# Kernel tuning notes

Hardware: AMD Instinct MI355X
Metric: run time of the kernel (lower is better)

Reference implementation:

```python
import jax, jax.numpy as jnp
import numpy as np

B, S, E = 2, 2048, 2048
H = 16
D = E // H  # head_dim = 128
ROPE_BASE = 10000.0


def _rope(x):
    # x: [B, H, S, D], rotate-half RoPE with offset=0
    half = D // 2
    inv_freq = 1.0 / (ROPE_BASE ** (jnp.arange(0, half, dtype=jnp.float32) * 2.0 / D))
    pos = jnp.arange(x.shape[2], dtype=jnp.float32)
    ang = pos[:, None] * inv_freq[None, :]          # [S, D/2]
    cos = jnp.cos(ang)[None, None, :, :]
    sin = jnp.sin(ang)[None, None, :, :]
    x1, x2 = x[..., :half], x[..., half:]
    return jnp.concatenate([x1 * cos - x2 * sin, x1 * sin + x2 * cos], axis=-1)


def setup_inputs() -> dict:
    key = jax.random.key(0)
    ks = jax.random.split(key, 9)
    sc = 1.0 / np.sqrt(E)
    inp = {
        'x': jax.random.normal(ks[0], (B, S, E), dtype=jnp.float32),
        'wq': jax.random.normal(ks[1], (E, E), dtype=jnp.float32) * sc,
        'bq': jax.random.normal(ks[2], (E,), dtype=jnp.float32) * 0.01,
        'wk': jax.random.normal(ks[3], (E, E), dtype=jnp.float32) * sc,
        'bk': jax.random.normal(ks[4], (E,), dtype=jnp.float32) * 0.01,
        'wv': jax.random.normal(ks[5], (E, E), dtype=jnp.float32) * sc,
        'bv': jax.random.normal(ks[6], (E,), dtype=jnp.float32) * 0.01,
        'wo': jax.random.normal(ks[7], (E, E), dtype=jnp.float32) * sc,
        'bo': jax.random.normal(ks[8], (E,), dtype=jnp.float32) * 0.01,
        'causal_mask': jnp.triu(jnp.ones((S, S), dtype=bool), k=1),  # True = masked
        'attention_mask': jnp.zeros((B, S), dtype=bool),             # True = padding
    }
    return inp


def reference(x, wq, bq, wk, bk, wv, bv, wo, bo, causal_mask, attention_mask):
    # nn.Linear: y = x @ W.T + b
    q = (x @ wq.T + bq).reshape(B, S, H, D).transpose(0, 2, 1, 3)  # [B,H,S,D]
    k = (x @ wk.T + bk).reshape(B, S, H, D).transpose(0, 2, 1, 3)
    v = (x @ wv.T + bv).reshape(B, S, H, D).transpose(0, 2, 1, 3)
    q = _rope(q)
    k = _rope(k)
    scores = jnp.einsum('bhsd,bhtd->bhst', q, k) / jnp.sqrt(jnp.float32(D))
    neg_inf = jnp.float32(-jnp.inf)
    scores = jnp.where(causal_mask[None, None, :, :], neg_inf, scores)
    scores = jnp.where(attention_mask[:, None, None, :], neg_inf, scores)
    attn = jax.nn.softmax(scores, axis=-1)
    out = jnp.einsum('bhst,bhtd->bhsd', attn, v)        # [B,H,S,D]
    out = out.transpose(0, 2, 1, 3).reshape(B, S, E)
    return out @ wo.T + bo
```

## Files before the change

### kernel.cpp

```cpp
#include <hip/hip_runtime.h>

#define BATCH 2
#define SEQ   2048
#define EMB   2048
#define NH    16
#define HD    128

typedef unsigned short u16;
typedef u16 u16x8 __attribute__((ext_vector_type(8)));
typedef __bf16 bf16x8 __attribute__((ext_vector_type(8)));
typedef float f32x4 __attribute__((ext_vector_type(4)));

__device__ __forceinline__ u16 f2bf(float f) {
  union { float f; unsigned u; } v; v.f = f;
  unsigned r = v.u + 0x7FFFu + ((v.u >> 16) & 1u);
  return (u16)(r >> 16);
}
__device__ __forceinline__ float bf2f(u16 b) {
  union { unsigned u; float f; } v; v.u = ((unsigned)b) << 16;
  return v.f;
}
__device__ __forceinline__ void gload_lds16(const u16* g, u16* l) {
  __builtin_amdgcn_global_load_lds(
      (__attribute__((address_space(1))) void*)(void*)g,
      (__attribute__((address_space(3))) void*)(void*)l, 16, 0, 0);
}

__global__ void cvt_f32_bf16(const float* __restrict__ in, u16* __restrict__ out, int n) {
  int i = (blockIdx.x * 256 + threadIdx.x) * 4;
  const int stride = gridDim.x * 256 * 4;
  for (; i + 3 < n; i += stride) {
    float4 v = *(const float4*)(in + i);
    u16 o0 = f2bf(v.x), o1 = f2bf(v.y), o2 = f2bf(v.z), o3 = f2bf(v.w);
    unsigned lo = (unsigned)o0 | ((unsigned)o1 << 16);
    unsigned hi = (unsigned)o2 | ((unsigned)o3 << 16);
    uint2 pack; pack.x = lo; pack.y = hi;
    *(uint2*)(out + i) = pack;
  }
}

__global__ void rope_table(float* __restrict__ cosT, float* __restrict__ sinT) {
  const int s = blockIdx.x;
  const int j = threadIdx.x;
  float inv = powf(10000.0f, -(float)j / 64.0f);
  float ang = (float)s * inv;
  cosT[s * 64 + j] = cosf(ang);
  sinT[s * 64 + j] = sinf(ang);
}

__global__ void rope_apply(u16* __restrict__ q, const float* __restrict__ cosT,
                           const float* __restrict__ sinT) {
  const int idx = blockIdx.x * 256 + threadIdx.x;
  const int j = idx & 63;
  const int s = (idx >> 6) & (SEQ - 1);
  const int bh = idx >> 17;
  u16* base = q + ((long)bh * SEQ + s) * HD;
  float x1 = bf2f(base[j]), x2 = bf2f(base[j + 64]);
  float c = cosT[s * 64 + j], sn = sinT[s * 64 + j];
  base[j]      = f2bf(x1 * c - x2 * sn);
  base[j + 64] = f2bf(x1 * sn + x2 * c);
}

__global__ __launch_bounds__(256)
void transpose_v(const u16* __restrict__ in, u16* __restrict__ out) {
  __shared__ u16 T[64 * 72];
  const int tid = threadIdx.x;
  const int s0 = blockIdx.x * 64, d0 = blockIdx.y * 64, bh = blockIdx.z;
  const int r = tid >> 2, c = tid & 3;
  const u16* ip = in + ((long)bh * SEQ + s0 + r) * HD + d0 + c * 16;
  *(u16x8*)&T[r * 72 + c * 16]     = *(const u16x8*)ip;
  *(u16x8*)&T[r * 72 + c * 16 + 8] = *(const u16x8*)(ip + 8);
  __syncthreads();
  u16* op = out + ((long)bh * HD + d0 + r) * SEQ + s0 + c * 16;
  u16x8 a, b;
#pragma unroll
  for (int e = 0; e < 8; ++e) a[e] = T[(c * 16 + e) * 72 + r];
#pragma unroll
  for (int e = 0; e < 8; ++e) b[e] = T[(c * 16 + 8 + e) * 72 + r];
  *(u16x8*)op = a;
  *(u16x8*)(op + 8) = b;
}

template <int MODE>
__global__ __launch_bounds__(256)
void gemm_bt(const u16* __restrict__ A, const u16* __restrict__ Bw,
             const float* __restrict__ bias, void* __restrict__ out,
             int M, int N, int K) {
  __shared__ u16 As[128 * 32];
  __shared__ u16 Bs[128 * 32];
  const int tid = threadIdx.x;
  const int wave = tid >> 6, lane = tid & 63;
  const int lr = lane & 15, lk = lane >> 4;
  const int m0 = blockIdx.y * 128, n0 = blockIdx.x * 128;
  const int wr = (wave >> 1) * 64, wc = (wave & 1) * 64;
  f32x4 acc[4][4] = {};
  for (int kt = 0; kt < K; kt += 32) {
#pragma unroll
    for (int c = 0; c < 2; ++c) {
      int idx = c * 256 + tid;
      int row = idx >> 2, col = (idx & 3) * 8;
      gload_lds16(A + (long)(m0 + row) * K + kt + col, As + idx * 8);
      gload_lds16(Bw + (long)(n0 + row) * K + kt + col, Bs + idx * 8);
    }
    __syncthreads();
    bf16x8 af[4], bfv[4];
#pragma unroll
    for (int m = 0; m < 4; ++m)
      af[m] = *(const bf16x8*)&As[(wr + m * 16 + lr) * 32 + lk * 8];
#pragma unroll
    for (int n = 0; n < 4; ++n)
      bfv[n] = *(const bf16x8*)&Bs[(wc + n * 16 + lr) * 32 + lk * 8];
#pragma unroll
    for (int m = 0; m < 4; ++m)
#pragma unroll
      for (int n = 0; n < 4; ++n)
        acc[m][n] = __builtin_amdgcn_mfma_f32_16x16x32_bf16(af[m], bfv[n], acc[m][n], 0, 0, 0);
    __syncthreads();
  }
#pragma unroll
  for (int n = 0; n < 4; ++n) {
    const int col = n0 + wc + n * 16 + lr;
    const float bb = bias[col];
#pragma unroll
    for (int m = 0; m < 4; ++m) {
      const int rbase = m0 + wr + m * 16 + lk * 4;
#pragma unroll
      for (int i = 0; i < 4; ++i) {
        const int row = rbase + i;
        const float val = acc[m][n][i] + bb;
        if (MODE == 0) {
          const int b = row >> 11, s = row & (SEQ - 1);
          const int h = col >> 7, d = col & (HD - 1);
          ((u16*)out)[(((long)(b * NH + h)) * SEQ + s) * HD + d] = f2bf(val);
        } else {
          ((float*)out)[(long)row * EMB + col] = val;
        }
      }
    }
  }
}

__global__ __launch_bounds__(256)
void attn_fwd(const u16* __restrict__ Q, const u16* __restrict__ K,
              const u16* __restrict__ Vt, u16* __restrict__ O) {
  __shared__ u16 Ks[64 * 128];
  __shared__ u16 Vts[128 * 64];
  __shared__ u16 Ps[4][16 * 72];
  const int tid = threadIdx.x, wave = tid >> 6, lane = tid & 63;
  const int lr = lane & 15, lk = lane >> 4;
  const int bh = blockIdx.y;
  const int qt = gridDim.x - 1 - blockIdx.x;
  const int qs = qt * 64;
  const long hoff = (long)bh * SEQ * HD;
  const u16* qb = Q + hoff + (long)(qs + wave * 16) * HD;

  bf16x8 qf[4];
#pragma unroll
  for (int ks = 0; ks < 4; ++ks)
    qf[ks] = *(const bf16x8*)(qb + (long)lr * HD + ks * 32 + lk * 8);

  f32x4 o[8] = {};
  float m_run[4] = {-1e30f, -1e30f, -1e30f, -1e30f};
  float l_run[4] = {0.f, 0.f, 0.f, 0.f};
  const float scale = 0.08838834764831845f;

  for (int t0 = 0; t0 <= qs; t0 += 64) {
#pragma unroll
    for (int c = 0; c < 4; ++c) {
      int i = c * 256 + tid;
      int row = i >> 4, cc = i & 15;
      int sc_ = cc ^ (row & 7);
      gload_lds16(K + hoff + (long)(t0 + row) * HD + sc_ * 8, Ks + i * 8);
    }
#pragma unroll
    for (int c = 0; c < 4; ++c) {
      int i = c * 256 + tid;
      int row = i >> 3, cc = i & 7;
      int sc_ = cc ^ (row & 7);
      gload_lds16(Vt + hoff + (long)row * SEQ + t0 + sc_ * 8, Vts + i * 8);
    }
    __syncthreads();

    f32x4 sc[4] = {};
#pragma unroll
    for (int tc = 0; tc < 4; ++tc) {
      const int rr = tc * 16 + lr;
#pragma unroll
      for (int ks = 0; ks < 4; ++ks) {
        bf16x8 kb = *(const bf16x8*)&Ks[rr * 128 + (((ks << 2) + lk) ^ (lr & 7)) * 8];
        sc[tc] = __builtin_amdgcn_mfma_f32_16x16x32_bf16(qf[ks], kb, sc[tc], 0, 0, 0);
      }
    }

    const bool diag = (t0 == qs);
    float rmax[4] = {-1e30f, -1e30f, -1e30f, -1e30f};
#pragma unroll
    for (int tc = 0; tc < 4; ++tc)
#pragma unroll
      for (int i = 0; i < 4; ++i) {
        float v = sc[tc][i] * scale;
        if (diag) {
          int tg = t0 + tc * 16 + lr;
          int qg = qs + wave * 16 + lk * 4 + i;
          if (tg > qg) v = -1e30f;
        }
        sc[tc][i] = v;
        rmax[i] = fmaxf(rmax[i], v);
      }
#pragma unroll
    for (int off = 1; off < 16; off <<= 1)
#pragma unroll
      for (int i = 0; i < 4; ++i)
        rmax[i] = fmaxf(rmax[i], __shfl_xor(rmax[i], off, 64));

    float alpha[4], rsum[4];
#pragma unroll
    for (int i = 0; i < 4; ++i) {
      float mn = fmaxf(m_run[i], rmax[i]);
      alpha[i] = __expf(m_run[i] - mn);
      m_run[i] = mn;
      rsum[i] = 0.f;
    }
#pragma unroll
    for (int tc = 0; tc < 4; ++tc)
#pragma unroll
      for (int i = 0; i < 4; ++i) {
        float p = __expf(sc[tc][i] - m_run[i]);
        sc[tc][i] = p;
        rsum[i] += p;
      }
#pragma unroll
    for (int off = 1; off < 16; off <<= 1)
#pragma unroll
      for (int i = 0; i < 4; ++i)
        rsum[i] += __shfl_xor(rsum[i], off, 64);
#pragma unroll
    for (int i = 0; i < 4; ++i) l_run[i] = l_run[i] * alpha[i] + rsum[i];
#pragma unroll
    for (int dc = 0; dc < 8; ++dc)
#pragma unroll
      for (int i = 0; i < 4; ++i) o[dc][i] *= alpha[i];

    u16* pw = Ps[wave];
#pragma unroll
    for (int tc = 0; tc < 4; ++tc)
#pragma unroll
      for (int i = 0; i < 4; ++i)
        pw[(lk * 4 + i) * 72 + tc * 16 + lr] = f2bf(sc[tc][i]);
    asm volatile("s_waitcnt lgkmcnt(0)" ::: "memory");

#pragma unroll
    for (int ks2 = 0; ks2 < 2; ++ks2) {
      bf16x8 pa = *(const bf16x8*)&pw[lr * 72 + ks2 * 32 + lk * 8];
#pragma unroll
      for (int dc = 0; dc < 8; ++dc) {
        const int dv = dc * 16 + lr;
        bf16x8 vb = *(const bf16x8*)&Vts[dv * 64 + (((ks2 << 2) + lk) ^ (lr & 7)) * 8];
        o[dc] = __builtin_amdgcn_mfma_f32_16x16x32_bf16(pa, vb, o[dc], 0, 0, 0);
      }
    }
    __syncthreads();
  }

  const int b = bh >> 4, h = bh & 15;
#pragma unroll
  for (int i = 0; i < 4; ++i) {
    float inv = 1.0f / l_run[i];
    int s = qs + wave * 16 + lk * 4 + i;
    u16* orow = O + ((long)b * SEQ + s) * EMB + h * HD;
#pragma unroll
    for (int dc = 0; dc < 8; ++dc)
      orow[dc * 16 + lr] = f2bf(o[dc][i] * inv);
  }
}

extern "C" void kernel_launch(void* const* d_in, const int* in_sizes, int n_in,
                              void* d_out, int out_size, void* d_ws, size_t ws_size,
                              hipStream_t stream) {
  const float* x  = (const float*)d_in[0];
  const float* wq = (const float*)d_in[1];
  const float* bq = (const float*)d_in[2];
  const float* wk = (const float*)d_in[3];
  const float* bk = (const float*)d_in[4];
  const float* wv = (const float*)d_in[5];
  const float* bv = (const float*)d_in[6];
  const float* wo = (const float*)d_in[7];
  const float* bo = (const float*)d_in[8];
  float* out = (float*)d_out;

  char* ws = (char*)d_ws;
  u16* xb  = (u16*)(ws + 0);
  u16* wqb = (u16*)(ws + 16777216);
  u16* wkb = (u16*)(ws + 25165824);
  u16* wvb = (u16*)(ws + 33554432);
  u16* wob = (u16*)(ws + 41943040);
  u16* qr  = (u16*)(ws + 50331648);
  u16* kr  = (u16*)(ws + 67108864);
  u16* vr  = (u16*)(ws + 83886080);
  u16* ao  = (u16*)(ws + 100663296);
  float* cosT = (float*)(ws + 117440512);
  float* sinT = (float*)(ws + 117964800);
  u16* vtr = xb;

  cvt_f32_bf16<<<2048, 256, 0, stream>>>(x, xb, BATCH * SEQ * EMB);
  cvt_f32_bf16<<<1024, 256, 0, stream>>>(wq, wqb, EMB * EMB);
  cvt_f32_bf16<<<1024, 256, 0, stream>>>(wk, wkb, EMB * EMB);
  cvt_f32_bf16<<<1024, 256, 0, stream>>>(wv, wvb, EMB * EMB);
  cvt_f32_bf16<<<1024, 256, 0, stream>>>(wo, wob, EMB * EMB);
  rope_table<<<SEQ, 64, 0, stream>>>(cosT, sinT);

  dim3 gg(EMB / 128, (BATCH * SEQ) / 128);
  gemm_bt<0><<<gg, 256, 0, stream>>>(xb, wqb, bq, qr, BATCH * SEQ, EMB, EMB);
  gemm_bt<0><<<gg, 256, 0, stream>>>(xb, wkb, bk, kr, BATCH * SEQ, EMB, EMB);
  gemm_bt<0><<<gg, 256, 0, stream>>>(xb, wvb, bv, vr, BATCH * SEQ, EMB, EMB);

  rope_apply<<<(BATCH * NH * SEQ * 64) / 256, 256, 0, stream>>>(qr, cosT, sinT);
  rope_apply<<<(BATCH * NH * SEQ * 64) / 256, 256, 0, stream>>>(kr, cosT, sinT);

  transpose_v<<<dim3(SEQ / 64, HD / 64, BATCH * NH), 256, 0, stream>>>(vr, vtr);

  attn_fwd<<<dim3(SEQ / 64, BATCH * NH), 256, 0, stream>>>(qr, kr, vtr, ao);

  gemm_bt<1><<<gg, 256, 0, stream>>>(ao, wob, bo, out, BATCH * SEQ, EMB, EMB);
}
```

Before: 601.5 us.

## Fuse QKV GEMMs and restructure attention with double buffering and lazy rescale

```diff
diff --git a/kernel.cpp b/kernel.cpp
--- a/kernel.cpp
+++ b/kernel.cpp
@@ -12,9 +12,8 @@
 typedef float f32x4 __attribute__((ext_vector_type(4)));
 
 __device__ __forceinline__ u16 f2bf(float f) {
-  union { float f; unsigned u; } v; v.f = f;
-  unsigned r = v.u + 0x7FFFu + ((v.u >> 16) & 1u);
-  return (u16)(r >> 16);
+  __bf16 h = (__bf16)f;
+  return __builtin_bit_cast(u16, h);
 }
 __device__ __forceinline__ float bf2f(u16 b) {
   union { unsigned u; float f; } v; v.u = ((unsigned)b) << 16;
@@ -84,7 +83,9 @@
 template <int MODE>
 __global__ __launch_bounds__(256)
 void gemm_bt(const u16* __restrict__ A, const u16* __restrict__ Bw,
-             const float* __restrict__ bias, void* __restrict__ out,
+             const float* __restrict__ b0, const float* __restrict__ b1,
+             const float* __restrict__ b2,
+             void* __restrict__ o0, void* __restrict__ o1, void* __restrict__ o2,
              int M, int N, int K) {
   __shared__ u16 As[128 * 32];
   __shared__ u16 Bs[128 * 32];
@@ -120,7 +121,11 @@
 #pragma unroll
   for (int n = 0; n < 4; ++n) {
     const int col = n0 + wc + n * 16 + lr;
-    const float bb = bias[col];
+    const int which = col >> 11;
+    const float* bias = (which == 0) ? b0 : (which == 1) ? b1 : b2;
+    const int cc = col & (EMB - 1);
+    const float bb = bias[cc];
+    void* outp = (which == 0) ? o0 : (which == 1) ? o1 : o2;
 #pragma unroll
     for (int m = 0; m < 4; ++m) {
       const int rbase = m0 + wr + m * 16 + lk * 4;
@@ -130,148 +135,177 @@
         const float val = acc[m][n][i] + bb;
         if (MODE == 0) {
           const int b = row >> 11, s = row & (SEQ - 1);
-          const int h = col >> 7, d = col & (HD - 1);
-          ((u16*)out)[(((long)(b * NH + h)) * SEQ + s) * HD + d] = f2bf(val);
+          const int h = cc >> 7, d = cc & (HD - 1);
+          ((u16*)outp)[(((long)(b * NH + h)) * SEQ + s) * HD + d] = f2bf(val);
         } else {
-          ((float*)out)[(long)row * EMB + col] = val;
+          ((float*)outp)[(long)row * EMB + col] = val;
         }
       }
     }
   }
+}
+
+#define THR_RAW 90.51f
+__device__ __forceinline__ void attn_tile(
+    const bf16x8 qf[4], f32x4 o[8], float m[4], float l[4],
+    const u16* __restrict__ Ksb, const u16* __restrict__ Vtsb,
+    u16* __restrict__ pw, int lr, int lk, int t0, int rowbase, bool diag) {
+  const float SC2 = 0.08838834764831845f * 1.4426950408889634f;
+  f32x4 sc[4] = {};
+#pragma unroll
+  for (int tc = 0; tc < 4; ++tc) {
+    const int rr = tc * 16 + lr;
+#pragma unroll
+    for (int ks = 0; ks < 4; ++ks) {
+      bf16x8 kb = *(const bf16x8*)&Ksb[rr * 128 + (((ks << 2) + lk) ^ (lr & 7)) * 8];
+      sc[tc] = __builtin_amdgcn_mfma_f32_16x16x32_bf16(qf[ks], kb, sc[tc], 0, 0, 0);
+    }
+  }
+  float rmax[4] = {-3e38f, -3e38f, -3e38f, -3e38f};
+#pragma unroll
+  for (int tc = 0; tc < 4; ++tc)
+#pragma unroll
+    for (int i = 0; i < 4; ++i) {
+      float v = sc[tc][i];
+      if (diag) {
+        int tg = t0 + tc * 16 + lr;
+        int qg = rowbase + lk * 4 + i;
+        if (tg > qg) v = -3e38f;
+        sc[tc][i] = v;
+      }
+      rmax[i] = fmaxf(rmax[i], v);
+    }
+#pragma unroll
+  for (int off = 1; off < 16; off <<= 1)
+#pragma unroll
+    for (int i = 0; i < 4; ++i)
+      rmax[i] = fmaxf(rmax[i], __shfl_xor(rmax[i], off, 64));
+
+  bool small = (rmax[0] <= m[0] + THR_RAW) && (rmax[1] <= m[1] + THR_RAW) &&
+               (rmax[2] <= m[2] + THR_RAW) && (rmax[3] <= m[3] + THR_RAW);
+  if (!__all(small)) {
+#pragma unroll
+    for (int i = 0; i < 4; ++i) {
+      float mn = fmaxf(m[i], rmax[i]);
+      float a = __builtin_amdgcn_exp2f((m[i] - mn) * SC2);
+      m[i] = mn;
+      l[i] *= a;
+#pragma unroll
+      for (int dc = 0; dc < 8; ++dc) o[dc][i] *= a;
+    }
+  }
+  float rsum[4] = {0.f, 0.f, 0.f, 0.f};
+#pragma unroll
+  for (int tc = 0; tc < 4; ++tc)
+#pragma unroll
+    for (int i = 0; i < 4; ++i) {
+      float p = __builtin_amdgcn_exp2f((sc[tc][i] - m[i]) * SC2);
+      sc[tc][i] = p;
+      rsum[i] += p;
+    }
+#pragma unroll
+  for (int off = 1; off < 16; off <<= 1)
+#pragma unroll
+    for (int i = 0; i < 4; ++i)
+      rsum[i] += __shfl_xor(rsum[i], off, 64);
+#pragma unroll
+  for (int i = 0; i < 4; ++i) l[i] += rsum[i];
+
+#pragma unroll
+  for (int tc = 0; tc < 4; ++tc)
+#pragma unroll
+    for (int i = 0; i < 4; ++i)
+      pw[(lk * 4 + i) * 72 + tc * 16 + lr] = f2bf(sc[tc][i]);
+  asm volatile("s_waitcnt lgkmcnt(0)" ::: "memory");
+#pragma unroll
+  for (int ks2 = 0; ks2 < 2; ++ks2) {
+    bf16x8 pa = *(const bf16x8*)&pw[lr * 72 + ks2 * 32 + lk * 8];
+#pragma unroll
+    for (int dc = 0; dc < 8; ++dc) {
+      const int dv = dc * 16 + lr;
+      bf16x8 vb = *(const bf16x8*)&Vtsb[dv * 64 + (((ks2 << 2) + lk) ^ (lr & 7)) * 8];
+      o[dc] = __builtin_amdgcn_mfma_f32_16x16x32_bf16(pa, vb, o[dc], 0, 0, 0);
+    }
+  }
+  asm volatile("s_waitcnt lgkmcnt(0)" ::: "memory");
 }
 
 __global__ __launch_bounds__(256)
 void attn_fwd(const u16* __restrict__ Q, const u16* __restrict__ K,
               const u16* __restrict__ Vt, u16* __restrict__ O) {
-  __shared__ u16 Ks[64 * 128];
-  __shared__ u16 Vts[128 * 64];
+  __shared__ u16 Ks[2][64 * 128];
+  __shared__ u16 Vts[2][128 * 64];
   __shared__ u16 Ps[4][16 * 72];
   const int tid = threadIdx.x, wave = tid >> 6, lane = tid & 63;
   const int lr = lane & 15, lk = lane >> 4;
   const int bh = blockIdx.y;
-  const int qt = gridDim.x - 1 - blockIdx.x;
-  const int qs = qt * 64;
+  const int qbi = gridDim.x - 1 - blockIdx.x;
+  const int q0 = qbi * 128;
   const long hoff = (long)bh * SEQ * HD;
-  const u16* qb = Q + hoff + (long)(qs + wave * 16) * HD;
-
-  bf16x8 qf[4];
-#pragma unroll
-  for (int ks = 0; ks < 4; ++ks)
-    qf[ks] = *(const bf16x8*)(qb + (long)lr * HD + ks * 32 + lk * 8);
-
-  f32x4 o[8] = {};
-  float m_run[4] = {-1e30f, -1e30f, -1e30f, -1e30f};
-  float l_run[4] = {0.f, 0.f, 0.f, 0.f};
-  const float scale = 0.08838834764831845f;
-
-  for (int t0 = 0; t0 <= qs; t0 += 64) {
-#pragma unroll
-    for (int c = 0; c < 4; ++c) {
-      int i = c * 256 + tid;
-      int row = i >> 4, cc = i & 15;
-      int sc_ = cc ^ (row & 7);
-      gload_lds16(K + hoff + (long)(t0 + row) * HD + sc_ * 8, Ks + i * 8);
-    }
-#pragma unroll
-    for (int c = 0; c < 4; ++c) {
-      int i = c * 256 + tid;
-      int row = i >> 3, cc = i & 7;
-      int sc_ = cc ^ (row & 7);
-      gload_lds16(Vt + hoff + (long)row * SEQ + t0 + sc_ * 8, Vts + i * 8);
-    }
+
+#define ATTN_STAGE(buf, tt0)                                                   \
+  do {                                                                         \
+    _Pragma("unroll") for (int c = 0; c < 4; ++c) {                            \
+      int i_ = c * 256 + tid;                                                  \
+      int kr_ = i_ >> 4, kc_ = i_ & 15;                                        \
+      gload_lds16(K + hoff + (long)((tt0) + kr_) * HD + (kc_ ^ (kr_ & 7)) * 8, \
+                  &Ks[buf][i_ * 8]);                                           \
+    }                                                                          \
+    _Pragma("unroll") for (int c = 0; c < 4; ++c) {                            \
+      int i_ = c * 256 + tid;                                                  \
+      int vr_ = i_ >> 3, vc_ = i_ & 7;                                         \
+      gload_lds16(Vt + hoff + (long)vr_ * SEQ + (tt0) + (vc_ ^ (vr_ & 7)) * 8, \
+                  &Vts[buf][i_ * 8]);                                          \
+    }                                                                          \
+  } while (0)
+
+  const int rbA = q0 + wave * 16;
+  const int rbB = q0 + 64 + wave * 16;
+  bf16x8 qfA[4], qfB[4];
+  {
+    const u16* qpA = Q + hoff + (long)rbA * HD + (long)lr * HD;
+    const u16* qpB = Q + hoff + (long)rbB * HD + (long)lr * HD;
+#pragma unroll
+    for (int ks = 0; ks < 4; ++ks) {
+      qfA[ks] = *(const bf16x8*)(qpA + ks * 32 + lk * 8);
+      qfB[ks] = *(const bf16x8*)(qpB + ks * 32 + lk * 8);
+    }
+  }
+
+  f32x4 oA[8] = {}, oB[8] = {};
+  float mA[4] = {-3e38f, -3e38f, -3e38f, -3e38f}, lA[4] = {0.f, 0.f, 0.f, 0.f};
+  float mB[4] = {-3e38f, -3e38f, -3e38f, -3e38f}, lB[4] = {0.f, 0.f, 0.f, 0.f};
+
+  const int nt = q0 / 64 + 2;
+  ATTN_STAGE(0, 0);
+  int cur = 0;
+  for (int ti = 0; ti < nt; ++ti) {
+    const int t0 = ti * 64;
     __syncthreads();
-
-    f32x4 sc[4] = {};
-#pragma unroll
-    for (int tc = 0; tc < 4; ++tc) {
-      const int rr = tc * 16 + lr;
-#pragma unroll
-      for (int ks = 0; ks < 4; ++ks) {
-        bf16x8 kb = *(const bf16x8*)&Ks[rr * 128 + (((ks << 2) + lk) ^ (lr & 7)) * 8];
-        sc[tc] = __builtin_amdgcn_mfma_f32_16x16x32_bf16(qf[ks], kb, sc[tc], 0, 0, 0);
-      }
-    }
-
-    const bool diag = (t0 == qs);
-    float rmax[4] = {-1e30f, -1e30f, -1e30f, -1e30f};
-#pragma unroll
-    for (int tc = 0; tc < 4; ++tc)
-#pragma unroll
-      for (int i = 0; i < 4; ++i) {
-        float v = sc[tc][i] * scale;
-        if (diag) {
-          int tg = t0 + tc * 16 + lr;
-          int qg = qs + wave * 16 + lk * 4 + i;
-          if (tg > qg) v = -1e30f;
-        }
-        sc[tc][i] = v;
-        rmax[i] = fmaxf(rmax[i], v);
-      }
-#pragma unroll
-    for (int off = 1; off < 16; off <<= 1)
-#pragma unroll
-      for (int i = 0; i < 4; ++i)
-        rmax[i] = fmaxf(rmax[i], __shfl_xor(rmax[i], off, 64));
-
-    float alpha[4], rsum[4];
-#pragma unroll
-    for (int i = 0; i < 4; ++i) {
-      float mn = fmaxf(m_run[i], rmax[i]);
-      alpha[i] = __expf(m_run[i] - mn);
-      m_run[i] = mn;
-      rsum[i] = 0.f;
-    }
-#pragma unroll
-    for (int tc = 0; tc < 4; ++tc)
-#pragma unroll
-      for (int i = 0; i < 4; ++i) {
-        float p = __expf(sc[tc][i] - m_run[i]);
-        sc[tc][i] = p;
-        rsum[i] += p;
-      }
-#pragma unroll
-    for (int off = 1; off < 16; off <<= 1)
-#pragma unroll
-      for (int i = 0; i < 4; ++i)
-        rsum[i] += __shfl_xor(rsum[i], off, 64);
-#pragma unroll
-    for (int i = 0; i < 4; ++i) l_run[i] = l_run[i] * alpha[i] + rsum[i];
-#pragma unroll
-    for (int dc = 0; dc < 8; ++dc)
-#pragma unroll
-      for (int i = 0; i < 4; ++i) o[dc][i] *= alpha[i];
-
+    if (ti + 1 < nt) ATTN_STAGE(cur ^ 1, t0 + 64);
     u16* pw = Ps[wave];
-#pragma unroll
-    for (int tc = 0; tc < 4; ++tc)
-#pragma unroll
-      for (int i = 0; i < 4; ++i)
-        pw[(lk * 4 + i) * 72 + tc * 16 + lr] = f2bf(sc[tc][i]);
-    asm volatile("s_waitcnt lgkmcnt(0)" ::: "memory");
-
-#pragma unroll
-    for (int ks2 = 0; ks2 < 2; ++ks2) {
-      bf16x8 pa = *(const bf16x8*)&pw[lr * 72 + ks2 * 32 + lk * 8];
-#pragma unroll
-      for (int dc = 0; dc < 8; ++dc) {
-        const int dv = dc * 16 + lr;
-        bf16x8 vb = *(const bf16x8*)&Vts[dv * 64 + (((ks2 << 2) + lk) ^ (lr & 7)) * 8];
-        o[dc] = __builtin_amdgcn_mfma_f32_16x16x32_bf16(pa, vb, o[dc], 0, 0, 0);
-      }
-    }
-    __syncthreads();
+    if (t0 <= q0)
+      attn_tile(qfA, oA, mA, lA, Ks[cur], Vts[cur], pw, lr, lk, t0, rbA, t0 == q0);
+    attn_tile(qfB, oB, mB, lB, Ks[cur], Vts[cur], pw, lr, lk, t0, rbB, t0 == q0 + 64);
+    cur ^= 1;
   }
 
   const int b = bh >> 4, h = bh & 15;
 #pragma unroll
   for (int i = 0; i < 4; ++i) {
-    float inv = 1.0f / l_run[i];
-    int s = qs + wave * 16 + lk * 4 + i;
-    u16* orow = O + ((long)b * SEQ + s) * EMB + h * HD;
-#pragma unroll
-    for (int dc = 0; dc < 8; ++dc)
-      orow[dc * 16 + lr] = f2bf(o[dc][i] * inv);
-  }
+    float invA = 1.0f / lA[i];
+    float invB = 1.0f / lB[i];
+    int sA = rbA + lk * 4 + i;
+    int sB = rbB + lk * 4 + i;
+    u16* orA = O + ((long)b * SEQ + sA) * EMB + h * HD;
+    u16* orB = O + ((long)b * SEQ + sB) * EMB + h * HD;
+#pragma unroll
+    for (int dc = 0; dc < 8; ++dc) {
+      orA[dc * 16 + lr] = f2bf(oA[dc][i] * invA);
+      orB[dc * 16 + lr] = f2bf(oB[dc][i] * invB);
+    }
+  }
+#undef ATTN_STAGE
 }
 
 extern "C" void kernel_launch(void* const* d_in, const int* in_sizes, int n_in,
@@ -289,37 +323,36 @@
   float* out = (float*)d_out;
 
   char* ws = (char*)d_ws;
-  u16* xb  = (u16*)(ws + 0);
-  u16* wqb = (u16*)(ws + 16777216);
-  u16* wkb = (u16*)(ws + 25165824);
-  u16* wvb = (u16*)(ws + 33554432);
-  u16* wob = (u16*)(ws + 41943040);
-  u16* qr  = (u16*)(ws + 50331648);
-  u16* kr  = (u16*)(ws + 67108864);
-  u16* vr  = (u16*)(ws + 83886080);
-  u16* ao  = (u16*)(ws + 100663296);
+  u16* xb    = (u16*)(ws + 0);
+  u16* wqkvb = (u16*)(ws + 16777216);
+  u16* wob   = (u16*)(ws + 41943040);
+  u16* qr    = (u16*)(ws + 50331648);
+  u16* kr    = (u16*)(ws + 67108864);
+  u16* vr    = (u16*)(ws + 83886080);
+  u16* ao    = (u16*)(ws + 100663296);
   float* cosT = (float*)(ws + 117440512);
   float* sinT = (float*)(ws + 117964800);
   u16* vtr = xb;
 
   cvt_f32_bf16<<<2048, 256, 0, stream>>>(x, xb, BATCH * SEQ * EMB);
-  cvt_f32_bf16<<<1024, 256, 0, stream>>>(wq, wqb, EMB * EMB);
-  cvt_f32_bf16<<<1024, 256, 0, stream>>>(wk, wkb, EMB * EMB);
-  cvt_f32_bf16<<<1024, 256, 0, stream>>>(wv, wvb, EMB * EMB);
+  cvt_f32_bf16<<<1024, 256, 0, stream>>>(wq, wqkvb, EMB * EMB);
+  cvt_f32_bf16<<<1024, 256, 0, stream>>>(wk, wqkvb + EMB * EMB, EMB * EMB);
+  cvt_f32_bf16<<<1024, 256, 0, stream>>>(wv, wqkvb + 2 * EMB * EMB, EMB * EMB);
   cvt_f32_bf16<<<1024, 256, 0, stream>>>(wo, wob, EMB * EMB);
   rope_table<<<SEQ, 64, 0, stream>>>(cosT, sinT);
 
-  dim3 gg(EMB / 128, (BATCH * SEQ) / 128);
-  gemm_bt<0><<<gg, 256, 0, stream>>>(xb, wqb, bq, qr, BATCH * SEQ, EMB, EMB);
-  gemm_bt<0><<<gg, 256, 0, stream>>>(xb, wkb, bk, kr, BATCH * SEQ, EMB, EMB);
-  gemm_bt<0><<<gg, 256, 0, stream>>>(xb, wvb, bv, vr, BATCH * SEQ, EMB, EMB);
+  dim3 gq(3 * EMB / 128, (BATCH * SEQ) / 128);
+  gemm_bt<0><<<gq, 256, 0, stream>>>(xb, wqkvb, bq, bk, bv, qr, kr, vr,
+                                     BATCH * SEQ, 3 * EMB, EMB);
 
   rope_apply<<<(BATCH * NH * SEQ * 64) / 256, 256, 0, stream>>>(qr, cosT, sinT);
   rope_apply<<<(BATCH * NH * SEQ * 64) / 256, 256, 0, stream>>>(kr, cosT, sinT);
 
   transpose_v<<<dim3(SEQ / 64, HD / 64, BATCH * NH), 256, 0, stream>>>(vr, vtr);
 
-  attn_fwd<<<dim3(SEQ / 64, BATCH * NH), 256, 0, stream>>>(qr, kr, vtr, ao);
-
-  gemm_bt<1><<<gg, 256, 0, stream>>>(ao, wob, bo, out, BATCH * SEQ, EMB, EMB);
-}
+  attn_fwd<<<dim3(SEQ / 128, BATCH * NH), 256, 0, stream>>>(qr, kr, vtr, ao);
+
+  dim3 go(EMB / 128, (BATCH * SEQ) / 128);
+  gemm_bt<1><<<go, 256, 0, stream>>>(ao, wob, bo, nullptr, nullptr, out, nullptr,
+                                     nullptr, BATCH * SEQ, EMB, EMB);
+}
```

New measurement: 646.6 us. 7.5% more time.
